# Optimization experiments

Hardware: AMD Instinct MI355X
Metric: run time of the kernel (lower is better)

## Reference

```python
import jax, jax.numpy as jnp
import numpy as np

N = 8192
IN_DIM = 512
OUT_DIM = 64
ALPHA = 0.2  # leaky relu negative slope
NEG_INF = -9e15


def setup_inputs() -> dict:
    key = jax.random.key(0)
    k1, k2, k3, k4 = jax.random.split(key, 4)
    h = jax.random.normal(k1, (N, IN_DIM), dtype=jnp.float32)
    adj = jax.random.randint(k2, (N, N), 0, 2, dtype=jnp.int32)
    # xavier-uniform-ish scale for params
    W = jax.random.normal(k3, (IN_DIM, OUT_DIM), dtype=jnp.float32) * (1.414 / np.sqrt(IN_DIM))
    a = jax.random.normal(k4, (2 * OUT_DIM, 1), dtype=jnp.float32) * (1.414 / np.sqrt(2 * OUT_DIM))
    return {"h": h, "adj": adj, "W": W, "a": a}


def reference(h, adj, W, a):
    Wh = h @ W                                   # [N, out]
    Wh1 = Wh @ a[:OUT_DIM]                       # [N, 1]
    Wh2 = Wh @ a[OUT_DIM:]                       # [N, 1]
    e = jax.nn.leaky_relu(Wh1 + Wh2.T, negative_slope=ALPHA)  # [N, N]
    att = jnp.where(adj > 0, e, jnp.float32(NEG_INF))
    att = jax.nn.softmax(att, axis=1)            # masked row softmax
    # dropout is identity in eval mode
    h_next = att @ Wh                            # [N, out]
    return jax.nn.elu(h_next)                    # concat=True path
```

## Files before the change

### kernel.cpp

```cpp
#include <hip/hip_runtime.h>
#include <hip/hip_bf16.h>

#define NN 8192
#define IND 512
#define OUTD 64
#define ALPHA_ 0.2f
#define LOG2E 1.4426950408889634f

typedef float f32x4 __attribute__((ext_vector_type(4)));
typedef short s16x8 __attribute__((ext_vector_type(8)));
typedef int   i32x4 __attribute__((ext_vector_type(4)));

static __device__ __forceinline__ short f2bf(float x) {
    __hip_bfloat16 b = __float2bfloat16(x);
    return *reinterpret_cast<short*>(&b);
}

__global__ __launch_bounds__(256) void k_wh(const float* __restrict__ h,
                                            const float* __restrict__ W,
                                            const float* __restrict__ a,
                                            __hip_bfloat16* __restrict__ whT,
                                            float* __restrict__ Wh1,
                                            float* __restrict__ Wh2) {
    __shared__ float hs[8 * IND];
    int tid = threadIdx.x;
    const f32x4* h4 = (const f32x4*)(h + (size_t)blockIdx.x * 8 * IND);
    f32x4* hs4 = (f32x4*)hs;
    #pragma unroll
    for (int t = 0; t < 4; ++t) hs4[tid + t * 256] = h4[tid + t * 256];
    __syncthreads();

    int w = tid >> 6, l = tid & 63;
    int g = l >> 4, lc = l & 15;
    int c4 = lc * 4;
    const float* hrow = hs + (w * 2) * IND;
    f32x4 acc0 = {0.f, 0.f, 0.f, 0.f};
    f32x4 acc1 = {0.f, 0.f, 0.f, 0.f};

    #pragma unroll 4
    for (int k0 = 0; k0 < 128; ++k0) {
        int k = k0 * 4 + g;
        f32x4 wv = *(const f32x4*)(W + k * OUTD + c4);
        float h0 = hrow[k];
        float h1 = hrow[IND + k];
        acc0[0] = fmaf(h0, wv[0], acc0[0]);
        acc0[1] = fmaf(h0, wv[1], acc0[1]);
        acc0[2] = fmaf(h0, wv[2], acc0[2]);
        acc0[3] = fmaf(h0, wv[3], acc0[3]);
        acc1[0] = fmaf(h1, wv[0], acc1[0]);
        acc1[1] = fmaf(h1, wv[1], acc1[1]);
        acc1[2] = fmaf(h1, wv[2], acc1[2]);
        acc1[3] = fmaf(h1, wv[3], acc1[3]);
    }

    #pragma unroll
    for (int e = 0; e < 4; ++e) {
        acc0[e] += __shfl_xor(acc0[e], 16, 64);
        acc0[e] += __shfl_xor(acc0[e], 32, 64);
        acc1[e] += __shfl_xor(acc1[e], 16, 64);
        acc1[e] += __shfl_xor(acc1[e], 32, 64);
    }

    int row0 = blockIdx.x * 8 + w * 2;
    if (g == 0) {
        #pragma unroll
        for (int e = 0; e < 4; ++e) {
            whT[(size_t)(c4 + e) * NN + row0]     = __float2bfloat16(acc0[e]);
            whT[(size_t)(c4 + e) * NN + row0 + 1] = __float2bfloat16(acc1[e]);
        }
    }

    float p10 = 0.f, p20 = 0.f, p11 = 0.f, p21 = 0.f;
    #pragma unroll
    for (int e = 0; e < 4; ++e) {
        float a1 = a[c4 + e], a2 = a[OUTD + c4 + e];
        p10 = fmaf(acc0[e], a1, p10);
        p20 = fmaf(acc0[e], a2, p20);
        p11 = fmaf(acc1[e], a1, p11);
        p21 = fmaf(acc1[e], a2, p21);
    }
    #pragma unroll
    for (int off = 1; off < 16; off <<= 1) {
        p10 += __shfl_xor(p10, off, 64);
        p20 += __shfl_xor(p20, off, 64);
        p11 += __shfl_xor(p11, off, 64);
        p21 += __shfl_xor(p21, off, 64);
    }
    if (l == 0) {
        Wh1[row0] = p10;     Wh2[row0] = p20;
        Wh1[row0 + 1] = p11; Wh2[row0 + 1] = p21;
    }
}

__global__ __launch_bounds__(256) void k_max(const float* __restrict__ Wh2,
                                             float* __restrict__ mx) {
    float m = -1e30f;
    for (int i = threadIdx.x; i < NN; i += 256) m = fmaxf(m, Wh2[i]);
    #pragma unroll
    for (int off = 1; off < 64; off <<= 1) m = fmaxf(m, __shfl_xor(m, off, 64));
    __shared__ float sm[4];
    if ((threadIdx.x & 63) == 0) sm[threadIdx.x >> 6] = m;
    __syncthreads();
    if (threadIdx.x == 0) *mx = fmaxf(fmaxf(sm[0], sm[1]), fmaxf(sm[2], sm[3]));
}

__global__ __launch_bounds__(512) void k_gat(const int* __restrict__ adj,
                                             const __hip_bfloat16* __restrict__ whT,
                                             const float* __restrict__ Wh1,
                                             const float* __restrict__ Wh2,
                                             const float* __restrict__ mxp,
                                             float* __restrict__ out) {
    int tid = threadIdx.x;
    int w   = tid >> 6;
    int l   = tid & 63;
    int lr  = l & 15;
    int grp = l >> 4;
    int ib  = blockIdx.x * 16;
    int row = ib + lr;

    float wh1r = Wh1[row];
    float mi = wh1r + *mxp;
    mi = fmaxf(mi, ALPHA_ * mi);
    float mc = mi * LOG2E;

    f32x4 acc0 = {0.f, 0.f, 0.f, 0.f};
    f32x4 acc1 = acc0, acc2 = acc0, acc3 = acc0;
    float lsum = 0.f;

    const int* ap = adj + (size_t)row * NN;
    const __hip_bfloat16* bp = whT + (size_t)lr * NN;
    int jbase = w * 32 + grp * 8;

#define LOADJ(J, AV0, AV1, W20, W21, B0, B1, B2, B3)           \
    AV0 = *(const i32x4*)(ap + (J));                           \
    AV1 = *(const i32x4*)(ap + (J) + 4);                       \
    W20 = *(const f32x4*)(Wh2 + (J));                          \
    W21 = *(const f32x4*)(Wh2 + (J) + 4);                      \
    B0  = *(const s16x8*)(bp + (J));                           \
    B1  = *(const s16x8*)(bp + (size_t)16 * NN + (J));         \
    B2  = *(const s16x8*)(bp + (size_t)32 * NN + (J));         \
    B3  = *(const s16x8*)(bp + (size_t)48 * NN + (J));

    i32x4 av0, av1;
    f32x4 w20, w21;
    s16x8 b0, b1, b2, b3;
    LOADJ(jbase, av0, av1, w20, w21, b0, b1, b2, b3)

    for (int it = 0; it < 32; ++it) {
        i32x4 nav0, nav1;
        f32x4 nw20, nw21;
        s16x8 nb0, nb1, nb2, nb3;
        if (it < 31) {
            int jn = (it + 1) * 256 + jbase;
            LOADJ(jn, nav0, nav1, nw20, nw21, nb0, nb1, nb2, nb3)
        }

        s16x8 af;
        #pragma unroll
        for (int e = 0; e < 4; ++e) {
            float x = wh1r + w20[e];
            x = fmaxf(x, ALPHA_ * x);
            float p = exp2f(fmaf(x, LOG2E, -mc));
            p = (av0[e] > 0) ? p : 0.f;
            lsum += p;
            af[e] = f2bf(p);
        }
        #pragma unroll
        for (int e = 0; e < 4; ++e) {
            float x = wh1r + w21[e];
            x = fmaxf(x, ALPHA_ * x);
            float p = exp2f(fmaf(x, LOG2E, -mc));
            p = (av1[e] > 0) ? p : 0.f;
            lsum += p;
            af[e + 4] = f2bf(p);
        }
        acc0 = __builtin_amdgcn_mfma_f32_16x16x32_bf16(af, b0, acc0, 0, 0, 0);
        acc1 = __builtin_amdgcn_mfma_f32_16x16x32_bf16(af, b1, acc1, 0, 0, 0);
        acc2 = __builtin_amdgcn_mfma_f32_16x16x32_bf16(af, b2, acc2, 0, 0, 0);
        acc3 = __builtin_amdgcn_mfma_f32_16x16x32_bf16(af, b3, acc3, 0, 0, 0);

        if (it < 31) {
            av0 = nav0; av1 = nav1;
            w20 = nw20; w21 = nw21;
            b0 = nb0; b1 = nb1; b2 = nb2; b3 = nb3;
        }
    }
#undef LOADJ

    lsum += __shfl_xor(lsum, 16, 64);
    lsum += __shfl_xor(lsum, 32, 64);

    __shared__ float lacc[8][16][65];
    __shared__ float lls[8][16];
    #pragma unroll
    for (int reg = 0; reg < 4; ++reg) {
        int rr = grp * 4 + reg;
        lacc[w][rr][lr]      = acc0[reg];
        lacc[w][rr][16 + lr] = acc1[reg];
        lacc[w][rr][32 + lr] = acc2[reg];
        lacc[w][rr][48 + lr] = acc3[reg];
    }
    if (l < 16) lls[w][l] = lsum;
    __syncthreads();

    #pragma unroll
    for (int t = 0; t < 2; ++t) {
        int idx = tid + t * 512;
        int rr = idx >> 6, c = idx & 63;
        float v = 0.f, ls = 0.f;
        #pragma unroll
        for (int ww = 0; ww < 8; ++ww) {
            v += lacc[ww][rr][c];
            ls += lls[ww][rr];
        }
        float hv = v / ls;
        out[(size_t)(ib + rr) * OUTD + c] = hv > 0.f ? hv : exp2f(hv * LOG2E) - 1.f;
    }
}

extern "C" void kernel_launch(void* const* d_in, const int* in_sizes, int n_in,
                              void* d_out, int out_size, void* d_ws, size_t ws_size,
                              hipStream_t stream) {
    const float* h   = (const float*)d_in[0];
    const int*   adj = (const int*)d_in[1];
    const float* W   = (const float*)d_in[2];
    const float* a   = (const float*)d_in[3];
    float* out = (float*)d_out;

    char* ws = (char*)d_ws;
    __hip_bfloat16*  whT = (__hip_bfloat16*)ws;
    float*           Wh1 = (float*)(ws + 1048576);
    float*           Wh2 = Wh1 + NN;
    float*           mx  = Wh2 + NN;

    k_wh<<<NN / 8, 256, 0, stream>>>(h, W, a, whT, Wh1, Wh2);
    k_max<<<1, 256, 0, stream>>>(Wh2, mx);
    k_gat<<<NN / 16, 512, 0, stream>>>(adj, whT, Wh1, Wh2, mx, out);
}
```

Measured before the change: 132.9 us.

## Stage adj tiles into LDS asynchronously and fold max into projection kernel

The adjacency rows are now streamed into a triple-buffered LDS ring using global_load_lds with a rotated layout, so lanes read the mask from shared memory instead of issuing strided per-row global loads. The separate max-reduction kernel is removed: the projection kernel pre-scales Wh1/Wh2 by log2e and updates a global max through an order-preserving uint atomicMax, with a memset to initialise it. Row sums are now produced by an extra MFMA against a vector of ones, which replaces the scalar accumulation and its shuffle reduction. This adds one barrier per iteration and one more MFMA, and the register prefetch of the B operand and Wh2 values is dropped.

```diff
diff --git a/kernel.cpp b/kernel.cpp
--- a/kernel.cpp
+++ b/kernel.cpp
@@ -10,18 +10,32 @@
 typedef float f32x4 __attribute__((ext_vector_type(4)));
 typedef short s16x8 __attribute__((ext_vector_type(8)));
 typedef int   i32x4 __attribute__((ext_vector_type(4)));
+typedef unsigned int uint;
 
 static __device__ __forceinline__ short f2bf(float x) {
     __hip_bfloat16 b = __float2bfloat16(x);
     return *reinterpret_cast<short*>(&b);
 }
+static __device__ __forceinline__ uint fenc(float f) {
+    uint u = __float_as_uint(f);
+    return (u & 0x80000000u) ? ~u : (u | 0x80000000u);
+}
+static __device__ __forceinline__ float fdec(uint k) {
+    uint u = (k & 0x80000000u) ? (k & 0x7FFFFFFFu) : ~k;
+    return __uint_as_float(u);
+}
+
+#define GLD_LDS16(g, d) \
+    __builtin_amdgcn_global_load_lds((const __attribute__((address_space(1))) int*)(g), \
+                                     (__attribute__((address_space(3))) int*)(d), 16, 0, 0)
 
 __global__ __launch_bounds__(256) void k_wh(const float* __restrict__ h,
                                             const float* __restrict__ W,
                                             const float* __restrict__ a,
                                             __hip_bfloat16* __restrict__ whT,
-                                            float* __restrict__ Wh1,
-                                            float* __restrict__ Wh2) {
+                                            float* __restrict__ Wh1s,
+                                            float* __restrict__ Wh2s,
+                                            uint* __restrict__ mxk) {
     __shared__ float hs[8 * IND];
     int tid = threadIdx.x;
     const f32x4* h4 = (const f32x4*)(h + (size_t)blockIdx.x * 8 * IND);
@@ -87,29 +101,24 @@
         p21 += __shfl_xor(p21, off, 64);
     }
     if (l == 0) {
-        Wh1[row0] = p10;     Wh2[row0] = p20;
-        Wh1[row0 + 1] = p11; Wh2[row0 + 1] = p21;
-    }
-}
-
-__global__ __launch_bounds__(256) void k_max(const float* __restrict__ Wh2,
-                                             float* __restrict__ mx) {
-    float m = -1e30f;
-    for (int i = threadIdx.x; i < NN; i += 256) m = fmaxf(m, Wh2[i]);
-    #pragma unroll
-    for (int off = 1; off < 64; off <<= 1) m = fmaxf(m, __shfl_xor(m, off, 64));
-    __shared__ float sm[4];
-    if ((threadIdx.x & 63) == 0) sm[threadIdx.x >> 6] = m;
-    __syncthreads();
-    if (threadIdx.x == 0) *mx = fmaxf(fmaxf(sm[0], sm[1]), fmaxf(sm[2], sm[3]));
+        float s20 = p20 * LOG2E, s21 = p21 * LOG2E;
+        Wh1s[row0]     = p10 * LOG2E;  Wh2s[row0]     = s20;
+        Wh1s[row0 + 1] = p11 * LOG2E;  Wh2s[row0 + 1] = s21;
+        atomicMax(mxk, fenc(fmaxf(s20, s21)));
+    }
 }
 
 __global__ __launch_bounds__(512) void k_gat(const int* __restrict__ adj,
                                              const __hip_bfloat16* __restrict__ whT,
-                                             const float* __restrict__ Wh1,
-                                             const float* __restrict__ Wh2,
-                                             const float* __restrict__ mxp,
+                                             const float* __restrict__ Wh1s,
+                                             const float* __restrict__ Wh2s,
+                                             const uint* __restrict__ mxk,
                                              float* __restrict__ out) {
+    __shared__ char smem[49152];
+    int (*sbuf)[16][256] = (int(*)[16][256])smem;
+    float (*lacc)[16][65] = (float(*)[16][65])smem;
+    float (*lls)[16] = (float(*)[16])(smem + 8 * 16 * 65 * 4);
+
     int tid = threadIdx.x;
     int w   = tid >> 6;
     int l   = tid & 63;
@@ -118,80 +127,77 @@
     int ib  = blockIdx.x * 16;
     int row = ib + lr;
 
-    float wh1r = Wh1[row];
-    float mi = wh1r + *mxp;
-    mi = fmaxf(mi, ALPHA_ * mi);
-    float mc = mi * LOG2E;
+    float wh1s = Wh1s[row];
+    float t0 = wh1s + fdec(*mxk);
+    float mcs = fmaxf(t0, ALPHA_ * t0);
 
     f32x4 acc0 = {0.f, 0.f, 0.f, 0.f};
-    f32x4 acc1 = acc0, acc2 = acc0, acc3 = acc0;
-    float lsum = 0.f;
-
-    const int* ap = adj + (size_t)row * NN;
+    f32x4 acc1 = acc0, acc2 = acc0, acc3 = acc0, acc4 = acc0;
+    s16x8 bones;
+    #pragma unroll
+    for (int e = 0; e < 8; ++e) bones[e] = (short)0x3F80;
+
+    int r0 = 2 * w, r1 = 2 * w + 1;
+    const int* g0 = adj + (size_t)(ib + r0) * NN + ((l * 4 - 8 * r0) & 255);
+    const int* g1 = adj + (size_t)(ib + r1) * NN + ((l * 4 - 8 * r1) & 255);
+
+    int w0 = w * 32 + grp * 8;
+    int p0 = (w0 + 8 * lr) & 255;
+    int p1 = (w0 + 4 + 8 * lr) & 255;
+
     const __hip_bfloat16* bp = whT + (size_t)lr * NN;
-    int jbase = w * 32 + grp * 8;
-
-#define LOADJ(J, AV0, AV1, W20, W21, B0, B1, B2, B3)           \
-    AV0 = *(const i32x4*)(ap + (J));                           \
-    AV1 = *(const i32x4*)(ap + (J) + 4);                       \
-    W20 = *(const f32x4*)(Wh2 + (J));                          \
-    W21 = *(const f32x4*)(Wh2 + (J) + 4);                      \
-    B0  = *(const s16x8*)(bp + (J));                           \
-    B1  = *(const s16x8*)(bp + (size_t)16 * NN + (J));         \
-    B2  = *(const s16x8*)(bp + (size_t)32 * NN + (J));         \
-    B3  = *(const s16x8*)(bp + (size_t)48 * NN + (J));
-
-    i32x4 av0, av1;
-    f32x4 w20, w21;
-    s16x8 b0, b1, b2, b3;
-    LOADJ(jbase, av0, av1, w20, w21, b0, b1, b2, b3)
+
+#define STAGE(b, itc) do {                                   \
+        GLD_LDS16(g0 + (size_t)(itc) * 256, &sbuf[b][r0][0]); \
+        GLD_LDS16(g1 + (size_t)(itc) * 256, &sbuf[b][r1][0]); \
+    } while (0)
+
+    STAGE(0, 0);
+    STAGE(1, 1);
 
     for (int it = 0; it < 32; ++it) {
-        i32x4 nav0, nav1;
-        f32x4 nw20, nw21;
-        s16x8 nb0, nb1, nb2, nb3;
-        if (it < 31) {
-            int jn = (it + 1) * 256 + jbase;
-            LOADJ(jn, nav0, nav1, nw20, nw21, nb0, nb1, nb2, nb3)
-        }
+        __syncthreads();
+        if (it < 30) STAGE((it + 2) % 3, it + 2);
+
+        const int* rb = &sbuf[it % 3][lr][0];
+        i32x4 a0 = *(const i32x4*)(rb + p0);
+        i32x4 a1 = *(const i32x4*)(rb + p1);
+
+        int jl = it * 256 + w0;
+        f32x4 w20 = *(const f32x4*)(Wh2s + jl);
+        f32x4 w21 = *(const f32x4*)(Wh2s + jl + 4);
+        s16x8 b0 = *(const s16x8*)(bp + jl);
+        s16x8 b1 = *(const s16x8*)(bp + (size_t)16 * NN + jl);
+        s16x8 b2 = *(const s16x8*)(bp + (size_t)32 * NN + jl);
+        s16x8 b3 = *(const s16x8*)(bp + (size_t)48 * NN + jl);
 
         s16x8 af;
         #pragma unroll
         for (int e = 0; e < 4; ++e) {
-            float x = wh1r + w20[e];
-            x = fmaxf(x, ALPHA_ * x);
-            float p = exp2f(fmaf(x, LOG2E, -mc));
-            p = (av0[e] > 0) ? p : 0.f;
-            lsum += p;
+            float t = wh1s + w20[e];
+            float x = fmaxf(t, ALPHA_ * t);
+            float p = exp2f(x - mcs);
+            p = (a0[e] != 0) ? p : 0.f;
             af[e] = f2bf(p);
         }
         #pragma unroll
         for (int e = 0; e < 4; ++e) {
-            float x = wh1r + w21[e];
-            x = fmaxf(x, ALPHA_ * x);
-            float p = exp2f(fmaf(x, LOG2E, -mc));
-            p = (av1[e] > 0) ? p : 0.f;
-            lsum += p;
+            float t = wh1s + w21[e];
+            float x = fmaxf(t, ALPHA_ * t);
+            float p = exp2f(x - mcs);
+            p = (a1[e] != 0) ? p : 0.f;
             af[e + 4] = f2bf(p);
         }
         acc0 = __builtin_amdgcn_mfma_f32_16x16x32_bf16(af, b0, acc0, 0, 0, 0);
         acc1 = __builtin_amdgcn_mfma_f32_16x16x32_bf16(af, b1, acc1, 0, 0, 0);
         acc2 = __builtin_amdgcn_mfma_f32_16x16x32_bf16(af, b2, acc2, 0, 0, 0);
         acc3 = __builtin_amdgcn_mfma_f32_16x16x32_bf16(af, b3, acc3, 0, 0, 0);
-
-        if (it < 31) {
-            av0 = nav0; av1 = nav1;
-            w20 = nw20; w21 = nw21;
-            b0 = nb0; b1 = nb1; b2 = nb2; b3 = nb3;
-        }
-    }
-#undef LOADJ
-
-    lsum += __shfl_xor(lsum, 16, 64);
-    lsum += __shfl_xor(lsum, 32, 64);
-
-    __shared__ float lacc[8][16][65];
-    __shared__ float lls[8][16];
+        acc4 = __builtin_amdgcn_mfma_f32_16x16x32_bf16(af, bones, acc4, 0, 0, 0);
+    }
+#undef STAGE
+
+    __syncthreads();
+
     #pragma unroll
     for (int reg = 0; reg < 4; ++reg) {
         int rr = grp * 4 + reg;
@@ -200,7 +206,10 @@
         lacc[w][rr][32 + lr] = acc2[reg];
         lacc[w][rr][48 + lr] = acc3[reg];
     }
-    if (l < 16) lls[w][l] = lsum;
+    if (lr == 0) {
+        #pragma unroll
+        for (int reg = 0; reg < 4; ++reg) lls[w][grp * 4 + reg] = acc4[reg];
+    }
     __syncthreads();
 
     #pragma unroll
@@ -228,12 +237,12 @@
     float* out = (float*)d_out;
 
     char* ws = (char*)d_ws;
-    __hip_bfloat16*  whT = (__hip_bfloat16*)ws;
-    float*           Wh1 = (float*)(ws + 1048576);
-    float*           Wh2 = Wh1 + NN;
-    float*           mx  = Wh2 + NN;
-
-    k_wh<<<NN / 8, 256, 0, stream>>>(h, W, a, whT, Wh1, Wh2);
-    k_max<<<1, 256, 0, stream>>>(Wh2, mx);
-    k_gat<<<NN / 16, 512, 0, stream>>>(adj, whT, Wh1, Wh2, mx, out);
-}
+    __hip_bfloat16*  whT  = (__hip_bfloat16*)ws;
+    float*           Wh1s = (float*)(ws + 1048576);
+    float*           Wh2s = Wh1s + NN;
+    uint*            mxk  = (uint*)(Wh2s + NN);
+
+    hipMemsetAsync(mxk, 0, 4, stream);
+    k_wh<<<NN / 8, 256, 0, stream>>>(h, W, a, whT, Wh1s, Wh2s, mxk);
+    k_gat<<<NN / 16, 512, 0, stream>>>(adj, whT, Wh1s, Wh2s, mxk, out);
+}
```

Result: slower. 161.4 us (+21.5%).
